# Optimization experiments

Hardware: AMD Instinct MI355X
Metric: run time of the kernel (lower is better)

The kernel has to match this reference:

```python
import jax, jax.numpy as jnp
import numpy as np
from jax import lax

S = 64        # num_sam_segments
B = 2
HIMG = 336    # full-res SAM segmap / painted map
HP = 24       # DINO patch grid (336/14)
CD = 768      # DINO feature channels
CM = 3072     # concatenated backbone channels (4 layers * 768)
RH = 48       # readout spatial size ceil(336/7)
HID = 128     # SPADE hidden_mlp_channels
EPS = 1e-12


def conv2d(x, w, b=None, pad=0):
    out = lax.conv_general_dilated(x, w, (1, 1), [(pad, pad), (pad, pad)],
                                   dimension_numbers=("NCHW", "OIHW", "NCHW"))
    if b is not None:
        out = out + b[None, :, None, None]
    return out


def paint_semantic_map(f_sem, segmap):
    # f_sem: (B, C, Hp, Wp) float; segmap: (B, H, W) int
    Bn, C, Hp, Wp = f_sem.shape
    H, W = segmap.shape[1:]
    # torch F.interpolate mode='nearest' downsample: src_idx = floor(dst_idx * in/out)
    iy = (jnp.arange(Hp) * H) // Hp
    ix = (jnp.arange(Wp) * W) // Wp
    seg_p = segmap[:, iy][:, :, ix]                      # (B, Hp, Wp)
    ids = jnp.clip(seg_p, 0, S - 1).reshape(Bn, -1)      # (B, Np)
    ids_off = (ids + jnp.arange(Bn)[:, None] * S).reshape(-1)
    flat = f_sem.transpose(0, 2, 3, 1).reshape(Bn * Hp * Wp, C)
    sums = jax.ops.segment_sum(flat, ids_off, num_segments=Bn * S)
    cnt = jax.ops.segment_sum(jnp.ones((Bn * Hp * Wp, 1), flat.dtype), ids_off,
                              num_segments=Bn * S)
    means = jnp.where(cnt > 0, sums / jnp.maximum(cnt, 1.0), 0.0).reshape(Bn, S, C)
    pix = jnp.clip(segmap, 0, S - 1)                     # (B, H, W)
    painted = means[jnp.arange(Bn)[:, None, None], pix]  # (B, H, W, C) gather
    return painted.transpose(0, 3, 1, 2)                 # (B, C, H, W)


def spade_ln(x, painted, ws, bs, wg, bg, wb, bb):
    # layer_norm over (C,H,W) per sample, no affine
    mean = jnp.mean(x, axis=(1, 2, 3), keepdims=True)
    var = jnp.mean((x - mean) ** 2, axis=(1, 2, 3), keepdims=True)
    xn = (x - mean) * lax.rsqrt(var + EPS)
    sem = jax.image.resize(painted, (x.shape[0], painted.shape[1], x.shape[2], x.shape[3]),
                           method="bilinear")
    h = jax.nn.relu(conv2d(sem, ws, bs, pad=1))
    gamma = conv2d(h, wg, bg, pad=1)
    beta = conv2d(h, wb, bb, pad=1)
    return xn * (1.0 + gamma) + beta


def setup_inputs() -> dict:
    key = jax.random.key(0)
    ks = jax.random.split(key, 16)
    n = lambda k, sh: jax.random.normal(k, sh, jnp.float32) * 0.02
    inp = {
        "x_main": jax.random.normal(ks[0], (B, CM, RH, RH), jnp.float32),
        "f_sem": jax.random.normal(ks[1], (B, CD, HP, HP), jnp.float32),
        "segmap": jax.random.randint(ks[2], (B, HIMG, HIMG), 0, S, jnp.int32),
    }
    i = 3
    for li, nf in enumerate([CM, 8, 16]):
        inp[f"ws{li}"] = n(ks[i], (HID, CD, 3, 3)); inp[f"bs{li}"] = jnp.zeros((HID,), jnp.float32)
        inp[f"wg{li}"] = n(ks[i + 1], (nf, HID, 3, 3)); inp[f"bg{li}"] = jnp.zeros((nf,), jnp.float32)
        inp[f"wb{li}"] = n(ks[i + 2], (nf, HID, 3, 3)); inp[f"bb{li}"] = jnp.zeros((nf,), jnp.float32)
        i += 3
    inp["w0"] = n(ks[12], (8, CM, 1, 1)); inp["bias0"] = jnp.zeros((8,), jnp.float32)
    inp["w1"] = n(ks[13], (16, 8, 1, 1)); inp["bias1"] = jnp.zeros((16,), jnp.float32)
    inp["w2"] = n(ks[14], (1, 16, 1, 1)); inp["bias2"] = jnp.zeros((1,), jnp.float32)
    return inp


def reference(x_main, f_sem, segmap,
              ws0, bs0, wg0, bg0, wb0, bb0,
              ws1, bs1, wg1, bg1, wb1, bb1,
              ws2, bs2, wg2, bg2, wb2, bb2,
              w0, bias0, w1, bias1, w2, bias2):
    painted = paint_semantic_map(f_sem, segmap)
    h = spade_ln(x_main, painted, ws0, bs0, wg0, bg0, wb0, bb0)
    h = jax.nn.softplus(conv2d(h, w0) + bias0[None, :, None, None])
    h = spade_ln(h, painted, ws1, bs1, wg1, bg1, wb1, bb1)
    h = jax.nn.softplus(conv2d(h, w1) + bias1[None, :, None, None])
    h = spade_ln(h, painted, ws2, bs2, wg2, bg2, wb2, bb2)
    h = jax.nn.softplus(conv2d(h, w2) + bias2[None, :, None, None])
    return h  # (B, 1, RH, RH)
```

## Files before the change

kernel.cpp:

```cpp
#include <hip/hip_runtime.h>
#include <hip/hip_bf16.h>

typedef __hip_bfloat16 bf16;
typedef __bf16 v8bf __attribute__((ext_vector_type(8)));
typedef float v4f __attribute__((ext_vector_type(4)));

#define PB 2304
#define PTOT 4608

__device__ __forceinline__ float b2f(bf16 x){ return __bfloat162float(x); }
__device__ __forceinline__ bf16 f2b(float x){ return __float2bfloat16(x); }
__device__ __forceinline__ float softplus_f(float x){
  return fmaxf(x, 0.f) + log1pf(expf(-fabsf(x)));
}
__device__ __forceinline__ float LD(const void* src, size_t i, int fl){
  return fl ? ((const float*)src)[i] : b2f(((const bf16*)src)[i]);
}

__device__ __forceinline__ void gload_lds16(const void* g, void* l){
  __builtin_amdgcn_global_load_lds(
      (const __attribute__((address_space(1))) void*)g,
      (__attribute__((address_space(3))) void*)l, 16, 0, 0);
}

__global__ __launch_bounds__(256) void k_sniff(const unsigned* __restrict__ x, int* __restrict__ flag,
                                               float* __restrict__ zp){
  int t = threadIdx.x;
  if (t < 128) zp[t] = 0.f;
  int cnt = 0;
  for (int i = t; i < 4096; i += 256){
    unsigned e = (x[i] >> 8) & 0x7F;
    if (e >= 0x38 && e <= 0x42) cnt++;
  }
  for (int off = 32; off; off >>= 1) cnt += __shfl_down(cnt, off, 64);
  __shared__ int sc[4];
  if ((t & 63) == 0) sc[t >> 6] = cnt;
  __syncthreads();
  if (t == 0) *flag = (sc[0]+sc[1]+sc[2]+sc[3] < 2048) ? 1 : 0;
}

__global__ __launch_bounds__(256) void k_cvt_small(
    const void* s4, const void* s10, const void* s16, const void* s6, const void* s8,
    const void* s12, const void* s14, const void* s18, const void* s20,
    const void* s21, const void* s22, const void* s23, const void* s24,
    const void* s25, const void* s26,
    float* __restrict__ dst, const int* __restrict__ flag, float* __restrict__ MB){
  int i = blockIdx.x*256 + threadIdx.x;
  if (i >= 40537) return;
  if (i >= 31321){ MB[i - 31321] = 0.f; return; }
  int fl = *flag;
  const void* src; size_t off;
  if      (i < 128)   { src = s4;  off = i; }
  else if (i < 256)   { src = s10; off = i - 128; }
  else if (i < 384)   { src = s16; off = i - 256; }
  else if (i < 3456)  { src = s6;  off = i - 384; }
  else if (i < 6528)  { src = s8;  off = i - 3456; }
  else if (i < 6536)  { src = s12; off = i - 6528; }
  else if (i < 6544)  { src = s14; off = i - 6536; }
  else if (i < 6560)  { src = s18; off = i - 6544; }
  else if (i < 6576)  { src = s20; off = i - 6560; }
  else if (i < 31152) { src = s21; off = i - 6576; }
  else if (i < 31160) { src = s22; off = i - 31152; }
  else if (i < 31288) { src = s23; off = i - 31160; }
  else if (i < 31304) { src = s24; off = i - 31288; }
  else if (i < 31320) { src = s25; off = i - 31304; }
  else                { src = s26; off = i - 31320; }
  dst[i] = LD(src, off, fl);
}

__global__ __launch_bounds__(256) void k_bcol(const float* __restrict__ SMALLF, float* __restrict__ BCOL){
  int t = threadIdx.x;
  const float* BG1 = SMALLF + 6528; const float* BB1 = SMALLF + 6536;
  const float* BG2 = SMALLF + 6544; const float* BB2 = SMALLF + 6560;
  const float* BB0 = SMALLF + 3456; const float* W0  = SMALLF + 6576;
  if (t < 8)       BCOL[t] = BG1[t];
  else if (t < 16) BCOL[t] = BB1[t-8];
  else if (t < 32) BCOL[t] = BG2[t-16];
  else if (t < 48) BCOL[t] = BB2[t-32];
  else if (t < 64) BCOL[t] = 0.f;
  float part[8] = {0,0,0,0,0,0,0,0};
  for (int c = t; c < 3072; c += 256){
    float bb = BB0[c];
    #pragma unroll
    for (int oc = 0; oc < 8; oc++) part[oc] += bb*W0[oc*3072 + c];
  }
  __shared__ float red[4][8];
  int wv = t >> 6, lane = t & 63;
  #pragma unroll
  for (int oc = 0; oc < 8; oc++){
    float v = part[oc];
    for (int off = 32; off; off >>= 1) v += __shfl_down(v, off, 64);
    if (lane == 0) red[wv][oc] = v;
  }
  __syncthreads();
  if (t < 8) BCOL[48 + t] = red[0][t] + red[1][t] + red[2][t] + red[3][t];
}

__global__ __launch_bounds__(256) void k_mbeta(const void* __restrict__ wb0, const int* __restrict__ flag,
                                               const float* __restrict__ w0f, float* __restrict__ MB){
  int jb = blockIdx.x, nb = blockIdx.y, t = threadIdx.x;
  int fl = *flag;
  int jl = t & 127, nh = t >> 7;
  int j = jb*128 + jl;
  int src = jl*9 + jb;
  float acc[8] = {0,0,0,0,0,0,0,0};
  int n0 = nb*128 + nh*64;
  for (int i = 0; i < 64; i++){
    int n = n0 + i;
    float wv = LD(wb0, (size_t)n*1152 + src, fl);
    #pragma unroll
    for (int oc = 0; oc < 8; oc++) acc[oc] += wv*w0f[oc*3072 + n];
  }
  #pragma unroll
  for (int oc = 0; oc < 8; oc++) atomicAdd(&MB[oc*1152 + j], acc[oc]);
}

__global__ __launch_bounds__(256) void k_wsm(const float* __restrict__ MB, bf16* __restrict__ WSMALL){
  int i = blockIdx.x*256 + threadIdx.x;
  if (i >= 9216) return;
  float v = MB[i];
  bf16 hi = f2b(v);
  WSMALL[48*1152 + i] = hi;
  WSMALL[56*1152 + i] = f2b(v - b2f(hi));
}

template<int ICW>
__global__ __launch_bounds__(256) void k_permW(const void* __restrict__ src, bf16* __restrict__ dst,
                                               int total, const int* __restrict__ flag){
  int idx = blockIdx.x*256 + threadIdx.x;
  if (idx >= total) return;
  int oc = idx / (9*ICW);
  int rr = idx % (9*ICW);
  int dyx = rr / ICW, ic = rr % ICW;
  size_t si = (size_t)(oc*ICW + ic)*9 + dyx;
  dst[idx] = f2b(LD(src, si, *flag));
}

__global__ __launch_bounds__(256) void k_seg_means(const void* __restrict__ f_sem, const int* __restrict__ flag,
                                                   const int* __restrict__ segmap,
                                                   float* __restrict__ means){
  int s = blockIdx.x, b = blockIdx.y, t = threadIdx.x;
  int fl = *flag;
  __shared__ int sid[576];
  for (int i = t; i < 576; i += 256){
    int y = i / 24, x = i % 24;
    int v = segmap[b*336*336 + (y*14)*336 + x*14];
    sid[i] = min(max(v, 0), 63);
  }
  __syncthreads();
  float a0=0.f, a1=0.f, a2=0.f; int cnt = 0;
  for (int i = 0; i < 576; i++){
    if (sid[i] == s){
      cnt++;
      a0 += LD(f_sem, (size_t)(b*768 + t      )*576 + i, fl);
      a1 += LD(f_sem, (size_t)(b*768 + t + 256)*576 + i, fl);
      a2 += LD(f_sem, (size_t)(b*768 + t + 512)*576 + i, fl);
    }
  }
  float inv = cnt > 0 ? 1.f/(float)cnt : 0.f;
  float* o = means + (size_t)(b*64 + s)*768;
  o[t] = a0*inv; o[t+256] = a1*inv; o[t+512] = a2*inv;
}

__global__ __launch_bounds__(256) void k_tt(const void* __restrict__ ws0, const void* __restrict__ ws1,
    const void* __restrict__ ws2, const int* __restrict__ flag,
    const float* __restrict__ means, bf16* __restrict__ WTT){
  int bx = blockIdx.x;
  int dyx = bx / 24, ocb = bx % 24;
  int b = blockIdx.y, t = threadIdx.x;
  int fl = *flag;
  int ocg0 = ocb*16;
  const void* wsrc; int ocl0 = ocg0;
  if (ocl0 < 128) wsrc = ws0;
  else if (ocl0 < 256){ wsrc = ws1; ocl0 -= 128; }
  else { wsrc = ws2; ocl0 -= 256; }
  __shared__ float wl[16][768];
  for (int ol = 0; ol < 16; ol++)
    for (int ic = t; ic < 768; ic += 256)
      wl[ol][ic] = LD(wsrc, (size_t)(ocl0 + ol)*6912 + (size_t)ic*9 + dyx, fl);
  __syncthreads();
  int s = t & 63, og = t >> 6;
  const float* mr = means + ((size_t)b*64 + s)*768;
  float acc[4] = {0.f, 0.f, 0.f, 0.f};
  for (int ic = 0; ic < 768; ic += 4){
    float4 m = *reinterpret_cast<const float4*>(mr + ic);
    #pragma unroll
    for (int k = 0; k < 4; k++){
      const float* w = &wl[og + k*4][ic];
      acc[k] += m.x*w[0] + m.y*w[1] + m.z*w[2] + m.w*w[3];
    }
  }
  #pragma unroll
  for (int k = 0; k < 4; k++){
    bf16 h = f2b(acc[k]);
    size_t base = ((size_t)(b*384 + ocg0 + og + k*4))*1152 + (size_t)dyx*128 + s;
    WTT[base] = h;
    WTT[base + 64] = h;
  }
}

__global__ __launch_bounds__(192) void k_A(const int* __restrict__ segmap, bf16* __restrict__ AHL){
  int blk = blockIdx.x;
  int b = blk / PB, rem = blk % PB, yo = rem / 48, xo = rem % 48;
  __shared__ float accs[64];
  int t = threadIdx.x;
  if (t < 64) accs[t] = 0.f;
  __syncthreads();
  if (t < 169){
    int ty = t / 13, tx = t % 13;
    int jy = 7*yo - 3 + ty, jx = 7*xo - 3 + tx;
    if (jy >= 0 && jy < 336 && jx >= 0 && jx < 336){
      int wy = 7 - abs(ty - 6), wx = 7 - abs(tx - 6);
      int sv = segmap[b*336*336 + jy*336 + jx];
      sv = min(max(sv, 0), 63);
      atomicAdd(&accs[sv], (float)(wy*wx));
    }
  }
  int sumy = 0, sumx = 0;
  for (int k = 0; k < 13; k++){
    int jy = 7*yo - 3 + k; if (jy >= 0 && jy < 336) sumy += 7 - abs(k - 6);
    int jx = 7*xo - 3 + k; if (jx >= 0 && jx < 336) sumx += 7 - abs(k - 6);
  }
  __syncthreads();
  if (t < 64){
    float v = accs[t] / (float)(sumy*sumx);
    bf16 hi = f2b(v);
    AHL[(size_t)blk*128 + t] = hi;
    AHL[(size_t)blk*128 + 64 + t] = f2b(v - b2f(hi));
  }
}

__global__ __launch_bounds__(256) void k_ln_partial(const void* __restrict__ x, const int* __restrict__ flag,
                                                    float2* __restrict__ part){
  int b = blockIdx.y, blk = blockIdx.x, t = threadIdx.x;
  int fl = *flag;
  size_t base = (size_t)b*7077888 + (size_t)blk*55296;
  float s = 0.f, sq = 0.f;
  for (int i = 0; i < 216; i++){
    float v = LD(x, base + t + i*256, fl);
    s += v; sq += v*v;
  }
  for (int off = 32; off; off >>= 1){ s += __shfl_down(s, off, 64); sq += __shfl_down(sq, off, 64); }
  __shared__ float ls[4], lq[4];
  int w = t >> 6, lane = t & 63;
  if (lane == 0){ ls[w] = s; lq[w] = sq; }
  __syncthreads();
  if (t == 0) part[b*128 + blk] = make_float2(ls[0]+ls[1]+ls[2]+ls[3], lq[0]+lq[1]+lq[2]+lq[3]);
}

__global__ void k_ln_final(const float2* __restrict__ part, float* __restrict__ stats){
  int b = blockIdx.x, t = threadIdx.x;
  float2 v = part[b*128 + t];
  float s = v.x, sq = v.y;
  for (int off = 32; off; off >>= 1){ s += __shfl_down(s, off, 64); sq += __shfl_down(sq, off, 64); }
  __shared__ float ls[2], lq[2];
  if ((t & 63) == 0){ ls[t>>6] = s; lq[t>>6] = sq; }
  __syncthreads();
  if (t == 0){
    s = ls[0]+ls[1]; sq = lq[0]+lq[1];
    const float N = 7077888.f;
    float mean = s/N; float var = sq/N - mean*mean; var = fmaxf(var, 0.f);
    stats[b*2] = mean; stats[b*2+1] = rsqrtf(var + 1e-12f);
  }
}

__global__ __launch_bounds__(256) void k_spln(float* __restrict__ z, int cnt, float* __restrict__ stats){
  int b = blockIdx.x, t = threadIdx.x;
  float* p = z + (size_t)b*cnt;
  float s = 0.f, sq = 0.f;
  for (int i = t; i < cnt; i += 256){
    float v = softplus_f(p[i]);
    p[i] = v;
    s += v; sq += v*v;
  }
  for (int off = 32; off; off >>= 1){ s += __shfl_down(s, off, 64); sq += __shfl_down(sq, off, 64); }
  __shared__ float ls[4], lq[4];
  int w = t >> 6, lane = t & 63;
  if (lane == 0){ ls[w] = s; lq[w] = sq; }
  __syncthreads();
  if (t == 0){
    s = ls[0]+ls[1]+ls[2]+ls[3]; sq = lq[0]+lq[1]+lq[2]+lq[3];
    float mean = s/(float)cnt; float var = sq/(float)cnt - mean*mean; var = fmaxf(var, 0.f);
    stats[b*2] = mean; stats[b*2+1] = rsqrtf(var + 1e-12f);
  }
}

__global__ __launch_bounds__(256) void k_ln_small(const float* __restrict__ z, int cnt, float* __restrict__ stats){
  int b = blockIdx.x, t = threadIdx.x;
  const float* p = z + (size_t)b*cnt;
  float s = 0.f, sq = 0.f;
  for (int i = t; i < cnt; i += 256){ float v = p[i]; s += v; sq += v*v; }
  for (int off = 32; off; off >>= 1){ s += __shfl_down(s, off, 64); sq += __shfl_down(sq, off, 64); }
  __shared__ float ls[4], lq[4];
  int w = t >> 6, lane = t & 63;
  if (lane == 0){ ls[w] = s; lq[w] = sq; }
  __syncthreads();
  if (t == 0){
    s = ls[0]+ls[1]+ls[2]+ls[3]; sq = lq[0]+lq[1]+lq[2]+lq[3];
    float mean = s/(float)cnt; float var = sq/(float)cnt - mean*mean; var = fmaxf(var, 0.f);
    stats[b*2] = mean; stats[b*2+1] = rsqrtf(var + 1e-12f);
  }
}

template<bool RELU, typename OT>
__device__ __forceinline__ void gemm_body(
    const bf16* __restrict__ Asrc, int AS, int acol, int ICW,
    const bf16* __restrict__ W, int K, size_t wbstride,
    const float* __restrict__ bp0, const float* __restrict__ bp1, const float* __restrict__ bp2, int seg,
    OT* __restrict__ out, int N, int ncb, int ldo, const bf16* __restrict__ zpad,
    int m0, int n0, bf16 (*Al)[64], bf16 (*Bl)[64])
{
  int t = threadIdx.x;
  int wv = t >> 6, lane = t & 63;
  int lr8 = lane >> 3, sseg = (lane & 7) ^ lr8;
  int b = m0 >= PB ? 1 : 0;

  int ya[2], xa[2]; bool bv[2]; const bf16* wb[2];
  #pragma unroll
  for (int i = 0; i < 2; i++){
    int sp = (m0 - b*PB) + wv*16 + i*8 + lr8;
    ya[i] = sp / 48; xa[i] = sp % 48;
    int nrow = ncb + n0 + wv*16 + i*8 + lr8;
    bv[i] = nrow < N;
    wb[i] = W + (size_t)b*wbstride + (size_t)nrow*K + sseg*8;
  }

  int wm = (wv >> 1)*32, wn = (wv & 1)*32;
  int lrow = lane & 15, quad = lane >> 4;
  int sx = lrow & 7;
  int o0 = ((quad    ) ^ sx)*8;
  int o1 = ((quad + 4) ^ sx)*8;

  v4f acc00 = {0,0,0,0}, acc01 = {0,0,0,0}, acc10 = {0,0,0,0}, acc11 = {0,0,0,0};

  int dyx = 0, ic0 = 0;
  int ktn = K / 64;
  for (int kt = 0; kt < ktn; kt++){
    int dy = dyx/3 - 1, dx = dyx%3 - 1;
    #pragma unroll
    for (int i = 0; i < 2; i++){
      int ys = ya[i] + dy, xs = xa[i] + dx;
      const bf16* ga = (ys >= 0 && ys < 48 && xs >= 0 && xs < 48)
        ? Asrc + (size_t)(b*PB + ys*48 + xs)*AS + acol + ic0 + sseg*8 : zpad;
      gload_lds16(ga, &Al[wv*16 + i*8][0]);
      const bf16* gb = bv[i] ? wb[i] + kt*64 : zpad;
      gload_lds16(gb, &Bl[wv*16 + i*8][0]);
    }
    asm volatile("s_waitcnt vmcnt(0)" ::: "memory");
    __syncthreads();
    v8bf a00 = *reinterpret_cast<const v8bf*>(&Al[wm      + lrow][o0]);
    v8bf a10 = *reinterpret_cast<const v8bf*>(&Al[wm + 16 + lrow][o0]);
    v8bf a01 = *reinterpret_cast<const v8bf*>(&Al[wm      + lrow][o1]);
    v8bf a11 = *reinterpret_cast<const v8bf*>(&Al[wm + 16 + lrow][o1]);
    v8bf b00 = *reinterpret_cast<const v8bf*>(&Bl[wn      + lrow][o0]);
    v8bf b10 = *reinterpret_cast<const v8bf*>(&Bl[wn + 16 + lrow][o0]);
    v8bf b01 = *reinterpret_cast<const v8bf*>(&Bl[wn      + lrow][o1]);
    v8bf b11 = *reinterpret_cast<const v8bf*>(&Bl[wn + 16 + lrow][o1]);
    acc00 = __builtin_amdgcn_mfma_f32_16x16x32_bf16(a00, b00, acc00, 0, 0, 0);
    acc00 = __builtin_amdgcn_mfma_f32_16x16x32_bf16(a01, b01, acc00, 0, 0, 0);
    acc01 = __builtin_amdgcn_mfma_f32_16x16x32_bf16(a00, b10, acc01, 0, 0, 0);
    acc01 = __builtin_amdgcn_mfma_f32_16x16x32_bf16(a01, b11, acc01, 0, 0, 0);
    acc10 = __builtin_amdgcn_mfma_f32_16x16x32_bf16(a10, b00, acc10, 0, 0, 0);
    acc10 = __builtin_amdgcn_mfma_f32_16x16x32_bf16(a11, b01, acc10, 0, 0, 0);
    acc11 = __builtin_amdgcn_mfma_f32_16x16x32_bf16(a10, b10, acc11, 0, 0, 0);
    acc11 = __builtin_amdgcn_mfma_f32_16x16x32_bf16(a11, b11, acc11, 0, 0, 0);
    __syncthreads();
    ic0 += 64; if (ic0 == ICW){ ic0 = 0; dyx++; }
  }

  auto store_tile = [&](v4f a, int mi, int ni){
    int gcol = ncb + n0 + wn + ni*16 + lrow;
    if (gcol >= N) return;
    int sel = gcol / seg; sel = sel > 2 ? 2 : sel;
    const float* bp = sel == 0 ? bp0 : (sel == 1 ? bp1 : bp2);
    float bias = bp[gcol - sel*seg];
    int rowb = m0 + wm + mi*16 + quad*4;
    #pragma unroll
    for (int rg = 0; rg < 4; rg++){
      float v = a[rg] + bias;
      if (RELU) v = fmaxf(v, 0.f);
      if constexpr (sizeof(OT) == 2) out[(size_t)(rowb+rg)*ldo + (gcol - ncb)] = f2b(v);
      else                           out[(size_t)(rowb+rg)*ldo + (gcol - ncb)] = (OT)v;
    }
  };
  store_tile(acc00, 0, 0); store_tile(acc01, 0, 1);
  store_tile(acc10, 1, 0); store_tile(acc11, 1, 1);
}

template<bool RELU, typename OT>
__global__ __launch_bounds__(256) void k_gemm(
    const bf16* __restrict__ Asrc, int AS, int acol, int ICW,
    const bf16* __restrict__ W, int K, size_t wbstride,
    const float* __restrict__ bp0, const float* __restrict__ bp1, const float* __restrict__ bp2, int seg,
    OT* __restrict__ out, int N, int ncb, int ldo, const bf16* __restrict__ zpad)
{
  __shared__ __align__(16) bf16 Al[64][64];
  __shared__ __align__(16) bf16 Bl[64][64];
  gemm_body<RELU, OT>(Asrc, AS, acol, ICW, W, K, wbstride, bp0, bp1, bp2, seg,
                      out, N, ncb, ldo, zpad, blockIdx.x*64, blockIdx.y*64, Al, Bl);
}

__global__ __launch_bounds__(256) void k_gsmall(
    const bf16* __restrict__ HS, const bf16* __restrict__ WSMALL, const float* __restrict__ BCOL,
    float* __restrict__ GBS, const bf16* __restrict__ zpad)
{
  __shared__ __align__(16) bf16 Al[64][64];
  __shared__ __align__(16) bf16 Bl[64][64];
  int y = blockIdx.y;
  int acol = y == 0 ? 128 : (y == 1 ? 256 : 0);
  const bf16* W = WSMALL + (y == 0 ? 0 : (y == 1 ? 16*1152 : 48*1152));
  const float* bp = BCOL + (y == 0 ? 0 : (y == 1 ? 16 : 48));
  float* out = GBS + (y == 0 ? 0 : (y == 1 ? 16 : 48));
  int N = y == 1 ? 32 : 16;
  gemm_body<false, float>(HS, 384, acol, 128, W, 1152, 0, bp, bp, bp, 9999,
                          out, N, 0, 64, zpad, blockIdx.x*64, 0, Al, Bl);
}

__global__ __launch_bounds__(256, 4) void k_gfuse(
    const bf16* __restrict__ HS, const bf16* __restrict__ WG0, const float* __restrict__ BG0,
    const void* __restrict__ x, const int* __restrict__ flag, const float* __restrict__ stats,
    const float* __restrict__ w0f, float* __restrict__ z0, const bf16* __restrict__ zpad)
{
  __shared__ __align__(16) char lds_raw[36096];
  bf16 (*Al)[64]  = (bf16(*)[64])lds_raw;
  bf16 (*Bl)[64]  = (bf16(*)[64])(lds_raw + 16384);
  float (*xl)[132] = (float(*)[132])lds_raw;
  float (*w0l)[64] = (float(*)[64])(lds_raw + 33792);
  float* bg0l = (float*)(lds_raw + 35840);

  int t = threadIdx.x;
  int m0 = blockIdx.x*128, n0 = blockIdx.y*64;
  int b = m0 >= PB ? 1 : 0;
  int fl = *flag;

  int wv = t >> 6, lane = t & 63;
  int lr8 = lane >> 3, sseg = (lane & 7) ^ lr8;
  int spbase = m0 - b*PB;

  int ya[4], xa[4];
  #pragma unroll
  for (int i = 0; i < 4; i++){
    int sp = spbase + wv*32 + i*8 + lr8;
    ya[i] = sp / 48; xa[i] = sp % 48;
  }
  const bf16* wgb = WG0 + (size_t)(n0 + wv*16 + lr8)*1152 + sseg*8;

  int wm = wv*32, lrow = lane & 15, quad = lane >> 4;
  int sx = lrow & 7;

  v4f acc[2][4];
  #pragma unroll
  for (int mi = 0; mi < 2; mi++)
    #pragma unroll
    for (int ni = 0; ni < 4; ni++) acc[mi][ni] = (v4f){0,0,0,0};

  for (int kt = 0; kt < 18; kt++){
    int dyx = kt >> 1, icr = (kt & 1) << 6;
    int dy = dyx/3 - 1, dx = dyx%3 - 1;
    #pragma unroll
    for (int i = 0; i < 4; i++){
      int ys = ya[i] + dy, xs = xa[i] + dx;
      const bf16* ga = (ys >= 0 && ys < 48 && xs >= 0 && xs < 48)
        ? HS + (size_t)(b*PB + ys*48 + xs)*384 + icr + sseg*8 : zpad;
      gload_lds16(ga, &Al[wv*32 + i*8][0]);
    }
    #pragma unroll
    for (int i = 0; i < 2; i++)
      gload_lds16(wgb + (size_t)(i*8)*1152 + dyx*128 + icr, &Bl[wv*16 + i*8][0]);
    asm volatile("s_waitcnt vmcnt(0)" ::: "memory");
    __syncthreads();
    #pragma unroll
    for (int kh = 0; kh < 2; kh++){
      int oa = ((kh*4 + quad) ^ sx)*8;
      v8bf a0 = *reinterpret_cast<const v8bf*>(&Al[wm      + lrow][oa]);
      v8bf a1 = *reinterpret_cast<const v8bf*>(&Al[wm + 16 + lrow][oa]);
      #pragma unroll
      for (int ni = 0; ni < 4; ni++){
        v8bf bn = *reinterpret_cast<const v8bf*>(&Bl[ni*16 + lrow][oa]);
        acc[0][ni] = __builtin_amdgcn_mfma_f32_16x16x32_bf16(a0, bn, acc[0][ni], 0, 0, 0);
        acc[1][ni] = __builtin_amdgcn_mfma_f32_16x16x32_bf16(a1, bn, acc[1][ni], 0, 0, 0);
      }
    }
    __syncthreads();
  }

  for (int i = t; i < 512; i += 256) w0l[i >> 6][i & 63] = w0f[(size_t)(i >> 6)*3072 + n0 + (i & 63)];
  if (t < 64) bg0l[t] = BG0[n0 + t];

  if (fl){
    const float* xp = (const float*)x + ((size_t)(b*3072 + n0))*2304 + spbase;
    #pragma unroll
    for (int it = 0; it < 8; it++){
      int idx = it*256 + t;
      int row = idx >> 5, c4 = (idx & 31)*4;
      float4 v = *reinterpret_cast<const float4*>(xp + (size_t)row*2304 + c4);
      *reinterpret_cast<float4*>(&xl[row][c4]) = v;
    }
  } else {
    const bf16* xp = (const bf16*)x + ((size_t)(b*3072 + n0))*2304 + spbase;
    #pragma unroll
    for (int it = 0; it < 4; it++){
      int idx = it*256 + t;
      int row = idx >> 4, c8 = (idx & 15)*8;
      v8bf v = *reinterpret_cast<const v8bf*>(xp + (size_t)row*2304 + c8);
      float4 f0, f1;
      f0.x = (float)v[0]; f0.y = (float)v[1]; f0.z = (float)v[2]; f0.w = (float)v[3];
      f1.x = (float)v[4]; f1.y = (float)v[5]; f1.z = (float)v[6]; f1.w = (float)v[7];
      *reinterpret_cast<float4*>(&xl[row][c8])     = f0;
      *reinterpret_cast<float4*>(&xl[row][c8 + 4]) = f1;
    }
  }
  __syncthreads();

  float mean = stats[b*2], rstd = stats[b*2+1];

  for (int og2 = 0; og2 < 2; og2++){
    float s[2][4][4];
    #pragma unroll
    for (int mi = 0; mi < 2; mi++)
      #pragma unroll
      for (int rg = 0; rg < 4; rg++)
        #pragma unroll
        for (int oc = 0; oc < 4; oc++) s[mi][rg][oc] = 0.f;
    #pragma unroll
    for (int mi = 0; mi < 2; mi++){
      int pl = wm + mi*16 + quad*4;
      #pragma unroll
      for (int nis = 0; nis < 4; nis++){
        int c = nis*16 + lrow;
        float bg = bg0l[c];
        float w0v[4];
        #pragma unroll
        for (int oc = 0; oc < 4; oc++) w0v[oc] = w0l[og2*4 + oc][c];
        #pragma unroll
        for (int rg = 0; rg < 4; rg++){
          float gv = acc[mi][nis][rg] + bg;
          float xn = (xl[c][pl + rg] - mean)*rstd;
          float tv = xn*(1.f + gv);
          #pragma unroll
          for (int oc = 0; oc < 4; oc++) s[mi][rg][oc] += tv*w0v[oc];
        }
      }
    }
    #pragma unroll
    for (int mi = 0; mi < 2; mi++){
      #pragma unroll
      for (int rg = 0; rg < 4; rg++)
        #pragma unroll
        for (int oc = 0; oc < 4; oc++){
          float v = s[mi][rg][oc];
          v += __shfl_xor(v, 1, 64);
          v += __shfl_xor(v, 2, 64);
          v += __shfl_xor(v, 4, 64);
          v += __shfl_xor(v, 8, 64);
          s[mi][rg][oc] = v;
        }
      if (lrow == 0){
        int p = m0 + wm + mi*16 + quad*4;
        #pragma unroll
        for (int rg = 0; rg < 4; rg++)
          #pragma unroll
          for (int oc = 0; oc < 4; oc++)
            atomicAdd(&z0[(size_t)(p + rg)*8 + og2*4 + oc], s[mi][rg][oc]);
      }
    }
  }
}

__global__ __launch_bounds__(256) void k_z0init(const float* __restrict__ b0f, const float* __restrict__ GBS,
                                                float* __restrict__ z0){
  int i = blockIdx.x*256 + threadIdx.x;
  if (i >= 36864) return;
  int p = i >> 3, oc = i & 7;
  z0[i] = b0f[oc] + GBS[(size_t)p*64 + 48 + oc] + GBS[(size_t)p*64 + 56 + oc];
}

__global__ __launch_bounds__(256) void k_F1(const float* __restrict__ z0, const float* __restrict__ GBS,
    const float* __restrict__ stats, const float* __restrict__ w1f, const float* __restrict__ b1f,
    float* __restrict__ z1){
  int p = blockIdx.x*256 + threadIdx.x;
  if (p >= PTOT) return;
  int b = p / PB;
  float mean = stats[b*2], rstd = stats[b*2+1];
  const float* zr = z0 + (size_t)p*8;
  const float* gr = GBS + (size_t)p*64;
  float yv[8];
  #pragma unroll
  for (int c = 0; c < 8; c++) yv[c] = (zr[c] - mean)*rstd*(1.f + gr[c]) + gr[8 + c];
  #pragma unroll
  for (int oc = 0; oc < 16; oc++){
    float s = b1f[oc];
    #pragma unroll
    for (int c = 0; c < 8; c++) s += yv[c]*w1f[oc*8 + c];
    z1[(size_t)p*16 + oc] = softplus_f(s);
  }
}

__global__ __launch_bounds__(256) void k_F2(const float* __restrict__ z1, const float* __restrict__ GBS,
    const float* __restrict__ stats, const float* __restrict__ w2f, const float* __restrict__ b2f,
    void* __restrict__ outp, const int* __restrict__ flag){
  int p = blockIdx.x*256 + threadIdx.x;
  if (p >= PTOT) return;
  int b = p / PB;
  float mean = stats[b*2], rstd = stats[b*2+1];
  const float* zr = z1 + (size_t)p*16;
  const float* gr = GBS + (size_t)p*64 + 16;
  float s = b2f[0];
  #pragma unroll
  for (int c = 0; c < 16; c++){
    float yv = (zr[c] - mean)*rstd*(1.f + gr[c]) + gr[16 + c];
    s += yv*w2f[c];
  }
  float r = softplus_f(s);
  if (*flag) ((float*)outp)[p] = r;
  else       ((bf16*)outp)[p] = f2b(r);
}

extern "C" void kernel_launch(void* const* d_in, const int* in_sizes, int n_in,
                              void* d_out, int out_size, void* d_ws, size_t ws_size,
                              hipStream_t stream){
  const void* x_main = d_in[0];
  const void* f_sem  = d_in[1];
  const int*  segmap = (const int*)d_in[2];

  char* ws = (char*)d_ws;
  size_t o = 0;
  auto alloc = [&](size_t bytes){ size_t r = o; o = (o + bytes + 255) & ~(size_t)255; return r; };
  float* MEANS = (float*)(ws + alloc(98304u*4));
  bf16*  AHL   = (bf16*) (ws + alloc(589824u*2));
  bf16*  WTT   = (bf16*) (ws + alloc(884736u*2));
  bf16*  WG0   = (bf16*) (ws + alloc(3538944u*2));
  bf16*  WSMALL= (bf16*) (ws + alloc(73728u*2));
  bf16*  HS    = (bf16*) (ws + alloc(1769472u*2));
  float* GBS   = (float*)(ws + alloc(294912u*4));
  float* Z0    = (float*)(ws + alloc(36864u*4));
  float* Z1    = (float*)(ws + alloc(73728u*4));
  float2* LNP  = (float2*)(ws + alloc(256u*8));
  float* STATS = (float*)(ws + alloc(16u*4));
  int*   FLAG  = (int*)  (ws + alloc(64u));
  float* SMALLF= (float*)(ws + alloc(31321u*4));
  float* MB    = (float*)(ws + alloc(9216u*4));
  float* BCOL  = (float*)(ws + alloc(64u*4));
  bf16*  ZPAD  = (bf16*) (ws + alloc(512u));

  float *BS0=SMALLF+0, *BS1=SMALLF+128, *BS2=SMALLF+256;
  float *BG0=SMALLF+384;
  float *W0=SMALLF+6576, *B0=SMALLF+31152;
  float *W1=SMALLF+31160, *B1=SMALLF+31288;
  float *W2=SMALLF+31304, *B2=SMALLF+31320;

  k_sniff<<<1, 256, 0, stream>>>((const unsigned*)x_main, FLAG, (float*)ZPAD);
  k_cvt_small<<<159, 256, 0, stream>>>(d_in[4], d_in[10], d_in[16], d_in[6], d_in[8],
      d_in[12], d_in[14], d_in[18], d_in[20], d_in[21], d_in[22], d_in[23], d_in[24],
      d_in[25], d_in[26], SMALLF, FLAG, MB);
  k_bcol<<<1, 256, 0, stream>>>(SMALLF, BCOL);
  k_mbeta<<<dim3(9,24), 256, 0, stream>>>(d_in[7], FLAG, W0, MB);
  k_wsm<<<36, 256, 0, stream>>>(MB, WSMALL);

  k_permW<128><<<dim3((3538944+255)/256),256, 0, stream>>>(d_in[5],  WG0,            3538944, FLAG);
  k_permW<128><<<dim3((9216+255)/256),   256, 0, stream>>>(d_in[11], WSMALL,           9216, FLAG);
  k_permW<128><<<dim3((9216+255)/256),   256, 0, stream>>>(d_in[13], WSMALL + 8*1152,  9216, FLAG);
  k_permW<128><<<dim3((18432+255)/256),  256, 0, stream>>>(d_in[17], WSMALL + 16*1152, 18432, FLAG);
  k_permW<128><<<dim3((18432+255)/256),  256, 0, stream>>>(d_in[19], WSMALL + 32*1152, 18432, FLAG);

  k_ln_partial<<<dim3(128,2), 256, 0, stream>>>(x_main, FLAG, LNP);
  k_ln_final<<<2, 128, 0, stream>>>(LNP, STATS);
  k_seg_means<<<dim3(64,2), 256, 0, stream>>>(f_sem, FLAG, segmap, MEANS);
  k_tt<<<dim3(216,2), 256, 0, stream>>>(d_in[3], d_in[9], d_in[15], FLAG, MEANS, WTT);
  k_A<<<PTOT, 192, 0, stream>>>(segmap, AHL);

  k_gemm<true, bf16><<<dim3(72,6), 256, 0, stream>>>(AHL, 128, 0, 128, WTT, 1152, (size_t)384*1152,
      BS0, BS1, BS2, 128, HS, 384, 0, 384, ZPAD);
  k_gsmall<<<dim3(72,3), 256, 0, stream>>>(HS, WSMALL, BCOL, GBS, ZPAD);

  k_z0init<<<144, 256, 0, stream>>>(B0, GBS, Z0);
  k_gfuse<<<dim3(36,48), 256, 0, stream>>>(HS, WG0, BG0, x_main, FLAG, STATS, W0, Z0, ZPAD);
  k_spln<<<2, 256, 0, stream>>>(Z0, 18432, STATS + 4);

  k_F1<<<18, 256, 0, stream>>>(Z0, GBS, STATS + 4, W1, B1, Z1);
  k_ln_small<<<2, 256, 0, stream>>>(Z1, 36864, STATS + 8);
  k_F2<<<18, 256, 0, stream>>>(Z1, GBS, STATS + 8, W2, B2, d_out, FLAG);
}
```

Before: 621.7 us.

## Split fused gamma GEMM and 1x1 conv, stage weight permutes through LDS

The fused gamma-GEMM plus 1x1-conv kernel becomes two kernels. A wider 128x128-tile MFMA GEMM writes gamma in bf16 to a new 28 MB workspace buffer, and a separate kernel reads it back with x to form the modulated activations and reduce into z0. The large weight permute and the SPADE shared-conv weight gather are also moved into LDS-staged kernels, so k_tt reads contiguous fp32 weights instead of stride-9 gathers. The split removes the atomics per 64-channel tile and gives the GEMM more reuse, at the cost of a large extra global write and read of the gamma tensor.

```diff
diff --git a/kernel.cpp b/kernel.cpp
--- a/kernel.cpp
+++ b/kernel.cpp
@@ -136,6 +136,39 @@
   dst[idx] = f2b(LD(src, si, *flag));
 }
 
+__global__ __launch_bounds__(256) void k_permoc(const void* __restrict__ src, bf16* __restrict__ dst,
+                                                const int* __restrict__ flag){
+  __shared__ float lds[4608];
+  int t = threadIdx.x;
+  size_t base = (size_t)blockIdx.x*4608;
+  int fl = *flag;
+  for (int i = t; i < 4608; i += 256) lds[i] = LD(src, base + i, fl);
+  __syncthreads();
+  for (int i = t; i < 4608; i += 256){
+    int ocl = i / 1152, r = i - ocl*1152;
+    int dyx = r >> 7, ic = r & 127;
+    dst[base + i] = f2b(lds[ocl*1152 + ic*9 + dyx]);
+  }
+}
+
+__global__ __launch_bounds__(256) void k_permws(const void* __restrict__ ws0, const void* __restrict__ ws1,
+                                                const void* __restrict__ ws2, const int* __restrict__ flag,
+                                                float* __restrict__ WSP){
+  __shared__ float lds[6912];
+  int t = threadIdx.x;
+  int oc = blockIdx.x;
+  int l = oc >> 7, ocl = oc & 127;
+  const void* src = l == 0 ? ws0 : (l == 1 ? ws1 : ws2);
+  int fl = *flag;
+  for (int i = t; i < 6912; i += 256) lds[i] = LD(src, (size_t)ocl*6912 + i, fl);
+  __syncthreads();
+  float* o = WSP + (size_t)oc*6912;
+  for (int i = t; i < 6912; i += 256){
+    int dyx = i / 768, ic = i - dyx*768;
+    o[i] = lds[ic*9 + dyx];
+  }
+}
+
 __global__ __launch_bounds__(256) void k_seg_means(const void* __restrict__ f_sem, const int* __restrict__ flag,
                                                    const int* __restrict__ segmap,
                                                    float* __restrict__ means){
@@ -162,22 +195,16 @@
   o[t] = a0*inv; o[t+256] = a1*inv; o[t+512] = a2*inv;
 }
 
-__global__ __launch_bounds__(256) void k_tt(const void* __restrict__ ws0, const void* __restrict__ ws1,
-    const void* __restrict__ ws2, const int* __restrict__ flag,
+__global__ __launch_bounds__(256) void k_tt(const float* __restrict__ WSP,
     const float* __restrict__ means, bf16* __restrict__ WTT){
   int bx = blockIdx.x;
   int dyx = bx / 24, ocb = bx % 24;
   int b = blockIdx.y, t = threadIdx.x;
-  int fl = *flag;
   int ocg0 = ocb*16;
-  const void* wsrc; int ocl0 = ocg0;
-  if (ocl0 < 128) wsrc = ws0;
-  else if (ocl0 < 256){ wsrc = ws1; ocl0 -= 128; }
-  else { wsrc = ws2; ocl0 -= 256; }
   __shared__ float wl[16][768];
   for (int ol = 0; ol < 16; ol++)
     for (int ic = t; ic < 768; ic += 256)
-      wl[ol][ic] = LD(wsrc, (size_t)(ocl0 + ol)*6912 + (size_t)ic*9 + dyx, fl);
+      wl[ol][ic] = WSP[(size_t)(ocg0 + ol)*6912 + (size_t)dyx*768 + ic];
   __syncthreads();
   int s = t & 63, og = t >> 6;
   const float* mr = means + ((size_t)b*64 + s)*768;
@@ -416,23 +443,15 @@
                           out, N, 0, 64, zpad, blockIdx.x*64, 0, Al, Bl);
 }
 
-__global__ __launch_bounds__(256, 4) void k_gfuse(
+__global__ __launch_bounds__(256, 4) void k_gg(
     const bf16* __restrict__ HS, const bf16* __restrict__ WG0, const float* __restrict__ BG0,
-    const void* __restrict__ x, const int* __restrict__ flag, const float* __restrict__ stats,
-    const float* __restrict__ w0f, float* __restrict__ z0, const bf16* __restrict__ zpad)
+    bf16* __restrict__ GAMMA, const bf16* __restrict__ zpad)
 {
-  __shared__ __align__(16) char lds_raw[36096];
-  bf16 (*Al)[64]  = (bf16(*)[64])lds_raw;
-  bf16 (*Bl)[64]  = (bf16(*)[64])(lds_raw + 16384);
-  float (*xl)[132] = (float(*)[132])lds_raw;
-  float (*w0l)[64] = (float(*)[64])(lds_raw + 33792);
-  float* bg0l = (float*)(lds_raw + 35840);
-
-  int t = threadIdx.x;
-  int m0 = blockIdx.x*128, n0 = blockIdx.y*64;
+  __shared__ __align__(16) bf16 Al[128][64];
+  __shared__ __align__(16) bf16 Bl[128][64];
+  int t = threadIdx.x;
+  int m0 = blockIdx.x*128, n0 = blockIdx.y*128;
   int b = m0 >= PB ? 1 : 0;
-  int fl = *flag;
-
   int wv = t >> 6, lane = t & 63;
   int lr8 = lane >> 3, sseg = (lane & 7) ^ lr8;
   int spbase = m0 - b*PB;
@@ -443,16 +462,16 @@
     int sp = spbase + wv*32 + i*8 + lr8;
     ya[i] = sp / 48; xa[i] = sp % 48;
   }
-  const bf16* wgb = WG0 + (size_t)(n0 + wv*16 + lr8)*1152 + sseg*8;
+  const bf16* wgb = WG0 + (size_t)(n0 + wv*32 + lr8)*1152 + sseg*8;
 
   int wm = wv*32, lrow = lane & 15, quad = lane >> 4;
   int sx = lrow & 7;
 
-  v4f acc[2][4];
+  v4f acc[2][8];
   #pragma unroll
   for (int mi = 0; mi < 2; mi++)
     #pragma unroll
-    for (int ni = 0; ni < 4; ni++) acc[mi][ni] = (v4f){0,0,0,0};
+    for (int ni = 0; ni < 8; ni++) acc[mi][ni] = (v4f){0,0,0,0};
 
   for (int kt = 0; kt < 18; kt++){
     int dyx = kt >> 1, icr = (kt & 1) << 6;
@@ -463,10 +482,8 @@
       const bf16* ga = (ys >= 0 && ys < 48 && xs >= 0 && xs < 48)
         ? HS + (size_t)(b*PB + ys*48 + xs)*384 + icr + sseg*8 : zpad;
       gload_lds16(ga, &Al[wv*32 + i*8][0]);
-    }
-    #pragma unroll
-    for (int i = 0; i < 2; i++)
-      gload_lds16(wgb + (size_t)(i*8)*1152 + dyx*128 + icr, &Bl[wv*16 + i*8][0]);
+      gload_lds16(wgb + (size_t)(i*8)*1152 + dyx*128 + icr, &Bl[wv*32 + i*8][0]);
+    }
     asm volatile("s_waitcnt vmcnt(0)" ::: "memory");
     __syncthreads();
     #pragma unroll
@@ -475,7 +492,7 @@
       v8bf a0 = *reinterpret_cast<const v8bf*>(&Al[wm      + lrow][oa]);
       v8bf a1 = *reinterpret_cast<const v8bf*>(&Al[wm + 16 + lrow][oa]);
       #pragma unroll
-      for (int ni = 0; ni < 4; ni++){
+      for (int ni = 0; ni < 8; ni++){
         v8bf bn = *reinterpret_cast<const v8bf*>(&Bl[ni*16 + lrow][oa]);
         acc[0][ni] = __builtin_amdgcn_mfma_f32_16x16x32_bf16(a0, bn, acc[0][ni], 0, 0, 0);
         acc[1][ni] = __builtin_amdgcn_mfma_f32_16x16x32_bf16(a1, bn, acc[1][ni], 0, 0, 0);
@@ -484,86 +501,66 @@
     __syncthreads();
   }
 
-  for (int i = t; i < 512; i += 256) w0l[i >> 6][i & 63] = w0f[(size_t)(i >> 6)*3072 + n0 + (i & 63)];
-  if (t < 64) bg0l[t] = BG0[n0 + t];
-
-  if (fl){
-    const float* xp = (const float*)x + ((size_t)(b*3072 + n0))*2304 + spbase;
-    #pragma unroll
-    for (int it = 0; it < 8; it++){
-      int idx = it*256 + t;
-      int row = idx >> 5, c4 = (idx & 31)*4;
-      float4 v = *reinterpret_cast<const float4*>(xp + (size_t)row*2304 + c4);
-      *reinterpret_cast<float4*>(&xl[row][c4]) = v;
-    }
-  } else {
-    const bf16* xp = (const bf16*)x + ((size_t)(b*3072 + n0))*2304 + spbase;
-    #pragma unroll
-    for (int it = 0; it < 4; it++){
-      int idx = it*256 + t;
-      int row = idx >> 4, c8 = (idx & 15)*8;
-      v8bf v = *reinterpret_cast<const v8bf*>(xp + (size_t)row*2304 + c8);
-      float4 f0, f1;
-      f0.x = (float)v[0]; f0.y = (float)v[1]; f0.z = (float)v[2]; f0.w = (float)v[3];
-      f1.x = (float)v[4]; f1.y = (float)v[5]; f1.z = (float)v[6]; f1.w = (float)v[7];
-      *reinterpret_cast<float4*>(&xl[row][c8])     = f0;
-      *reinterpret_cast<float4*>(&xl[row][c8 + 4]) = f1;
-    }
-  }
-  __syncthreads();
-
-  float mean = stats[b*2], rstd = stats[b*2+1];
-
-  for (int og2 = 0; og2 < 2; og2++){
-    float s[2][4][4];
-    #pragma unroll
-    for (int mi = 0; mi < 2; mi++)
+  #pragma unroll
+  for (int mi = 0; mi < 2; mi++){
+    int pr = m0 + wm + mi*16 + quad*4;
+    #pragma unroll
+    for (int ni = 0; ni < 8; ni++){
+      int gc = n0 + ni*16 + lrow;
+      float bg = BG0[gc];
       #pragma unroll
       for (int rg = 0; rg < 4; rg++)
-        #pragma unroll
-        for (int oc = 0; oc < 4; oc++) s[mi][rg][oc] = 0.f;
-    #pragma unroll
-    for (int mi = 0; mi < 2; mi++){
-      int pl = wm + mi*16 + quad*4;
+        GAMMA[(size_t)(pr + rg)*3072 + gc] = f2b(acc[mi][ni][rg] + bg);
+    }
+  }
+}
+
+__global__ __launch_bounds__(256) void k_zc(
+    const void* __restrict__ x, const bf16* __restrict__ GAMMA, const int* __restrict__ flag,
+    const float* __restrict__ stats, const float* __restrict__ w0f, float* __restrict__ z0)
+{
+  __shared__ bf16 gmT[64][66];
+  __shared__ float w0l[8][64];
+  __shared__ float red[4][64][8];
+  int t = threadIdx.x;
+  int p0 = blockIdx.x*64, cb = blockIdx.y;
+  int b = p0 / PB;
+  int spbase = p0 - b*PB;
+  int fl = *flag;
+  float mean = stats[b*2], rstd = stats[b*2+1];
+  int px = t & 63, cg = t >> 6;
+  int pxs = t >> 6, cl = t & 63;
+
+  float acc[8] = {0,0,0,0,0,0,0,0};
+  for (int ct = 0; ct < 6; ct++){
+    int c0 = cb*384 + ct*64;
+    #pragma unroll
+    for (int k = 0; k < 16; k++){
+      int p = pxs + k*4;
+      gmT[cl][p] = GAMMA[(size_t)(p0 + p)*3072 + c0 + cl];
+    }
+    for (int i = t; i < 512; i += 256) w0l[i >> 6][i & 63] = w0f[(size_t)(i >> 6)*3072 + c0 + (i & 63)];
+    __syncthreads();
+    #pragma unroll
+    for (int ci = 0; ci < 16; ci++){
+      int c = cg*16 + ci;
+      float xv = LD(x, ((size_t)(b*3072 + c0 + c))*2304 + spbase + px, fl);
+      float xn = (xv - mean)*rstd;
+      float tv = xn*(1.f + b2f(gmT[c][px]));
       #pragma unroll
-      for (int nis = 0; nis < 4; nis++){
-        int c = nis*16 + lrow;
-        float bg = bg0l[c];
-        float w0v[4];
-        #pragma unroll
-        for (int oc = 0; oc < 4; oc++) w0v[oc] = w0l[og2*4 + oc][c];
-        #pragma unroll
-        for (int rg = 0; rg < 4; rg++){
-          float gv = acc[mi][nis][rg] + bg;
-          float xn = (xl[c][pl + rg] - mean)*rstd;
-          float tv = xn*(1.f + gv);
-          #pragma unroll
-          for (int oc = 0; oc < 4; oc++) s[mi][rg][oc] += tv*w0v[oc];
-        }
-      }
-    }
-    #pragma unroll
-    for (int mi = 0; mi < 2; mi++){
-      #pragma unroll
-      for (int rg = 0; rg < 4; rg++)
-        #pragma unroll
-        for (int oc = 0; oc < 4; oc++){
-          float v = s[mi][rg][oc];
-          v += __shfl_xor(v, 1, 64);
-          v += __shfl_xor(v, 2, 64);
-          v += __shfl_xor(v, 4, 64);
-          v += __shfl_xor(v, 8, 64);
-          s[mi][rg][oc] = v;
-        }
-      if (lrow == 0){
-        int p = m0 + wm + mi*16 + quad*4;
-        #pragma unroll
-        for (int rg = 0; rg < 4; rg++)
-          #pragma unroll
-          for (int oc = 0; oc < 4; oc++)
-            atomicAdd(&z0[(size_t)(p + rg)*8 + og2*4 + oc], s[mi][rg][oc]);
-      }
-    }
+      for (int oc = 0; oc < 8; oc++) acc[oc] += tv*w0l[oc][c];
+    }
+    __syncthreads();
+  }
+  #pragma unroll
+  for (int oc = 0; oc < 8; oc++) red[cg][px][oc] = acc[oc];
+  __syncthreads();
+  #pragma unroll
+  for (int j = 0; j < 2; j++){
+    int idx = t + j*256;
+    int p2 = idx >> 3, o2 = idx & 7;
+    float s = red[0][p2][o2] + red[1][p2][o2] + red[2][p2][o2] + red[3][p2][o2];
+    atomicAdd(&z0[(size_t)(p0 + p2)*8 + o2], s);
   }
 }
 
@@ -632,6 +629,8 @@
   bf16*  WG0   = (bf16*) (ws + alloc(3538944u*2));
   bf16*  WSMALL= (bf16*) (ws + alloc(73728u*2));
   bf16*  HS    = (bf16*) (ws + alloc(1769472u*2));
+  float* WSP   = (float*)(ws + alloc(2654208u*4));
+  bf16*  GAMMA = (bf16*) (ws + alloc(14155776u*2));
   float* GBS   = (float*)(ws + alloc(294912u*4));
   float* Z0    = (float*)(ws + alloc(36864u*4));
   float* Z1    = (float*)(ws + alloc(73728u*4));
@@ -657,7 +656,8 @@
   k_mbeta<<<dim3(9,24), 256, 0, stream>>>(d_in[7], FLAG, W0, MB);
   k_wsm<<<36, 256, 0, stream>>>(MB, WSMALL);
 
-  k_permW<128><<<dim3((3538944+255)/256),256, 0, stream>>>(d_in[5],  WG0,            3538944, FLAG);
+  k_permoc<<<768, 256, 0, stream>>>(d_in[5], WG0, FLAG);
+  k_permws<<<384, 256, 0, stream>>>(d_in[3], d_in[9], d_in[15], FLAG, WSP);
   k_permW<128><<<dim3((9216+255)/256),   256, 0, stream>>>(d_in[11], WSMALL,           9216, FLAG);
   k_permW<128><<<dim3((9216+255)/256),   256, 0, stream>>>(d_in[13], WSMALL + 8*1152,  9216, FLAG);
   k_permW<128><<<dim3((18432+255)/256),  256, 0, stream>>>(d_in[17], WSMALL + 16*1152, 18432, FLAG);
@@ -666,7 +666,7 @@
   k_ln_partial<<<dim3(128,2), 256, 0, stream>>>(x_main, FLAG, LNP);
   k_ln_final<<<2, 128, 0, stream>>>(LNP, STATS);
   k_seg_means<<<dim3(64,2), 256, 0, stream>>>(f_sem, FLAG, segmap, MEANS);
-  k_tt<<<dim3(216,2), 256, 0, stream>>>(d_in[3], d_in[9], d_in[15], FLAG, MEANS, WTT);
+  k_tt<<<dim3(216,2), 256, 0, stream>>>(WSP, MEANS, WTT);
   k_A<<<PTOT, 192, 0, stream>>>(segmap, AHL);
 
   k_gemm<true, bf16><<<dim3(72,6), 256, 0, stream>>>(AHL, 128, 0, 128, WTT, 1152, (size_t)384*1152,
@@ -674,7 +674,8 @@
   k_gsmall<<<dim3(72,3), 256, 0, stream>>>(HS, WSMALL, BCOL, GBS, ZPAD);
 
   k_z0init<<<144, 256, 0, stream>>>(B0, GBS, Z0);
-  k_gfuse<<<dim3(36,48), 256, 0, stream>>>(HS, WG0, BG0, x_main, FLAG, STATS, W0, Z0, ZPAD);
+  k_gg<<<dim3(36,24), 256, 0, stream>>>(HS, WG0, BG0, GAMMA, ZPAD);
+  k_zc<<<dim3(72,8), 256, 0, stream>>>(x_main, GAMMA, FLAG, STATS, W0, Z0);
   k_spln<<<2, 256, 0, stream>>>(Z0, 18432, STATS + 4);
 
   k_F1<<<18, 256, 0, stream>>>(Z0, GBS, STATS + 4, W1, B1, Z1);
```

Measured after the change: 597.9 us. 1.04x faster.
